# Kernel optimization log

Measured on AMD Instinct MI355X. Metric: run time of the kernel, lower is better.

Reference implementation:

```python
import jax, jax.numpy as jnp
import numpy as np

N_NODES = 50000   # hypergraph nodes
N_EDGES = 20000   # hyperedges
M = 400000        # node-edge incidences (node copies)
L = 800000        # inner GIN graph edges per side
HID = 128
IN_DIM = 128
B = 32            # graphs in batch
C = 10            # num_classes
N_LAYERS = 2
INNER = 2         # inner_num_layers
BN_EPS = 1e-5


def setup_inputs() -> dict:
    key = jax.random.key(0)
    ks = jax.random.split(key, 16)
    s = 0.05
    inp = {}
    inp["x_N"] = jax.random.normal(ks[0], (N_NODES, IN_DIM), jnp.float32)
    # embedding linear
    inp["We"] = jax.random.normal(ks[1], (IN_DIM, HID), jnp.float32) * s
    inp["be"] = jnp.zeros((HID,), jnp.float32)
    # GIN params: [outer_layer, direction(N2E/E2N), inner_conv, mlp_linear, hid, hid]
    inp["Wg"] = jax.random.normal(ks[2], (N_LAYERS, 2, INNER, 2, HID, HID), jnp.float32) * s
    inp["bg"] = jnp.zeros((N_LAYERS, 2, INNER, 2, HID), jnp.float32)
    inp["eps_g"] = jnp.zeros((N_LAYERS, 2, INNER), jnp.float32)
    # eval-mode BatchNorm affine params per inner conv
    inp["gamma"] = jnp.ones((N_LAYERS, 2, INNER, HID), jnp.float32)
    inp["beta"] = jnp.zeros((N_LAYERS, 2, INNER, HID), jnp.float32)
    # per-layer prediction heads
    inp["Wp"] = jax.random.normal(ks[3], (N_LAYERS + 1, HID, C), jnp.float32) * s
    inp["bp"] = jnp.zeros((N_LAYERS + 1, C), jnp.float32)
    # index tensors
    inp["ori_node_idx"] = jax.random.randint(ks[4], (M,), 0, N_NODES)
    inp["node2edge"] = jax.random.randint(ks[5], (M,), 0, N_EDGES)
    inp["edge_index_N"] = jax.random.randint(ks[6], (2, L), 0, M)
    inp["ori_edge_idx"] = jax.random.randint(ks[7], (M,), 0, N_EDGES)
    inp["edge2node"] = jax.random.randint(ks[8], (M,), 0, N_NODES)
    inp["edge_index_E"] = jax.random.randint(ks[9], (2, L), 0, M)
    inp["batch"] = jax.random.randint(ks[10], (M,), 0, B)
    return inp


def _gin(x, src, dst, Wg, bg, eps, gamma, beta):
    # GIN over the copy graph: h = MLP((1+eps)*x + sum_{j->i} x_j), BN (eval), ReLU between convs
    inv_std = 1.0 / jnp.sqrt(1.0 + BN_EPS)
    n = x.shape[0]
    for l in range(INNER):
        agg = jax.ops.segment_sum(x[src], dst, num_segments=n)
        h = (1.0 + eps[l]) * x + agg
        h = jax.nn.relu(h @ Wg[l, 0] + bg[l, 0])
        h = h @ Wg[l, 1] + bg[l, 1]
        h = gamma[l] * h * inv_std + beta[l]
        x = jax.nn.relu(h) if l < INNER - 1 else h
    return x


def reference(x_N, We, be, Wg, bg, eps_g, gamma, beta, Wp, bp,
              ori_node_idx, node2edge, edge_index_N,
              ori_edge_idx, edge2node, edge_index_E, batch):
    node_x = x_N @ We + be                       # [N, HID]
    xs = [node_x]
    for i in range(N_LAYERS):
        # node -> edge: gather copies, inner GIN, segment-sum pool over hyperedges
        nx = node_x[ori_node_idx]                # [M, HID]
        nx = _gin(nx, edge_index_N[0], edge_index_N[1],
                  Wg[i, 0], bg[i, 0], eps_g[i, 0], gamma[i, 0], beta[i, 0])
        edge_x = jax.ops.segment_sum(nx, node2edge, num_segments=N_EDGES)
        edge_x = jax.nn.relu(edge_x)             # EdgeUpdate (dropout off in eval)
        # edge -> node
        ex = edge_x[ori_edge_idx]                # [M, HID]
        ex = _gin(ex, edge_index_E[0], edge_index_E[1],
                  Wg[i, 1], bg[i, 1], eps_g[i, 1], gamma[i, 1], beta[i, 1])
        node_x = jax.ops.segment_sum(ex, edge2node, num_segments=N_NODES)
        node_x = jax.nn.relu(node_x)             # NodeUpdate
        xs.append(node_x)
    score = jnp.zeros((B, C), x_N.dtype)
    for i, x in enumerate(xs):
        pooled = jax.ops.segment_sum(x[ori_node_idx], batch, num_segments=B)
        score = score + pooled @ Wp[i] + bp[i]
    return score
```

## Files before the change

kernel.cpp:

```cpp
#include <hip/hip_runtime.h>
#include <hip/hip_bf16.h>

#define HID 128
static const int N_NODES = 50000;
static const int N_EDGES = 20000;
static const int M_COPIES = 400000;
static const int L_EDGES = 800000;
static const int NBATCH = 32;
static const int NCLS = 10;
#define INV_STD 0.9999950000374997f
#define IDX_CAP 384

typedef __attribute__((ext_vector_type(4))) float f32x4;
typedef __attribute__((ext_vector_type(8))) short short8;
typedef __attribute__((ext_vector_type(8))) unsigned short ushort8;
typedef __attribute__((ext_vector_type(4))) unsigned short u16x4;

__device__ __forceinline__ float bf2f(unsigned short u) {
    union { unsigned u; float f; } v; v.u = ((unsigned)u) << 16; return v.f;
}
__device__ __forceinline__ unsigned short f2bf(float f) {
    union { float f; unsigned u; } v; v.f = f;
    unsigned r = v.u + 0x7FFFu + ((v.u >> 16) & 1u);
    return (unsigned short)(r >> 16);
}
__device__ __forceinline__ void gatomic_add(float* p, float v) {
    unsafeAtomicAdd(p, v);
}

__device__ __forceinline__ unsigned short* xs_addr(unsigned short* Xs, int c, int r) {
    int byte = ((c * 64 + r) * 16) ^ ((c & 7) << 4);
    return (unsigned short*)((char*)Xs + byte);
}

__device__ __forceinline__ void stage8(const unsigned short* __restrict__ Wmat, int e,
                                       unsigned short* buf, int wave, int lane) {
    const char* g = (const char*)Wmat + ((size_t)e << 12) + (wave << 10) + (lane << 4);
    char* l = (char*)buf + (wave << 10);
    __builtin_amdgcn_global_load_lds(
        (const __attribute__((address_space(1))) unsigned int*)g,
        (__attribute__((address_space(3))) unsigned int*)l,
        16, 0, 0);
}

template<int N>
__device__ __forceinline__ void pipe_barrier() {
    if constexpr (N == 0) asm volatile("s_waitcnt vmcnt(0)" ::: "memory");
    else                  asm volatile("s_waitcnt vmcnt(1)" ::: "memory");
    __builtin_amdgcn_s_barrier();
    asm volatile("" ::: "memory");
}

__device__ __forceinline__ void mfma4(const unsigned short* Ws, const short8* xv,
                                      f32x4& a, int quad, int ln) {
#pragma unroll
    for (int kc = 0; kc < 4; ++kc) {
        short8 wa = *(const short8*)(Ws + (((kc * 4 + quad) * 16) + ln) * 8);
        a = __builtin_amdgcn_mfma_f32_16x16x32_bf16(wa, xv[kc], a, 0, 0, 0);
    }
}

__global__ __launch_bounds__(256) void prep_w(const float* __restrict__ We,
                                              const float* __restrict__ Wg,
                                              unsigned short* __restrict__ Wt) {
    int t = blockIdx.x * 256 + threadIdx.x;
    if (t >= 17 * 16384) return;
    int mat = t >> 14, rem = t & 16383;
    int h = rem >> 11, r2 = rem & 2047;
    int gg = r2 >> 7, r3 = r2 & 127;
    int n = r3 >> 3, j = r3 & 7;
    int k = gg * 8 + j, col = h * 16 + n;
    const float* src = (mat == 0) ? We : (Wg + (size_t)(mat - 1) * 16384);
    Wt[t] = f2bf(src[k * 128 + col]);
}

__global__ __launch_bounds__(256) void hist2_k(
    const int* __restrict__ iA, int nA, int* __restrict__ cA,
    const int* __restrict__ iB, int nB, int* __restrict__ cB) {
    int t = blockIdx.x * 256 + threadIdx.x;
    if (t < nA) atomicAdd(&cA[iA[t]], 1);
    if (t < nB) atomicAdd(&cB[iB[t]], 1);
}

__global__ __launch_bounds__(256) void scan1d_k(
    int* __restrict__ a0, int n0, int* __restrict__ p0,
    int* __restrict__ a1, int n1, int* __restrict__ p1) {
    int* a    = blockIdx.y ? a1 : a0;
    int n     = blockIdx.y ? n1 : n0;
    int* part = blockIdx.y ? p1 : p0;
    if ((int)(blockIdx.x * 256) >= n) return;
    __shared__ int s[256];
    int i = blockIdx.x * 256 + threadIdx.x;
    int v = (i < n) ? a[i] : 0;
    s[threadIdx.x] = v;
    __syncthreads();
#pragma unroll
    for (int d = 1; d < 256; d <<= 1) {
        int t = (threadIdx.x >= d) ? s[threadIdx.x - d] : 0;
        __syncthreads();
        s[threadIdx.x] += t;
        __syncthreads();
    }
    if (i < n) a[i] = s[threadIdx.x] - v;
    if (threadIdx.x == 255) part[blockIdx.x] = s[255];
}

__global__ __launch_bounds__(256) void scan2d_k(
    int* __restrict__ p0, int nb0, int* __restrict__ p1, int nb1) {
    int* part = blockIdx.x ? p1 : p0;
    int nb    = blockIdx.x ? nb1 : nb0;
    __shared__ int s[256];
    __shared__ int carry;
    if (threadIdx.x == 0) carry = 0;
    __syncthreads();
    for (int base = 0; base < nb; base += 256) {
        int i = base + threadIdx.x;
        int v = (i < nb) ? part[i] : 0;
        s[threadIdx.x] = v;
        __syncthreads();
#pragma unroll
        for (int d = 1; d < 256; d <<= 1) {
            int t = (threadIdx.x >= d) ? s[threadIdx.x - d] : 0;
            __syncthreads();
            s[threadIdx.x] += t;
            __syncthreads();
        }
        if (i < nb) part[i] = carry + s[threadIdx.x] - v;
        __syncthreads();
        if (threadIdx.x == 0) carry += s[255];
        __syncthreads();
    }
}

__global__ __launch_bounds__(256) void scan3d_k(
    int* __restrict__ a0, int n0, const int* __restrict__ p0,
    int* __restrict__ a1, int n1, const int* __restrict__ p1) {
    int* a          = blockIdx.y ? a1 : a0;
    int n           = blockIdx.y ? n1 : n0;
    const int* part = blockIdx.y ? p1 : p0;
    int i = blockIdx.x * 256 + threadIdx.x;
    if (i < n) a[i] += part[blockIdx.x];
}

__global__ __launch_bounds__(256) void fill_edge2_k(
    const int* __restrict__ sA, const int* __restrict__ dA, const int* __restrict__ rA,
    int nA, int* __restrict__ oA, int* __restrict__ ssA, int* __restrict__ ccA,
    const int* __restrict__ sB, const int* __restrict__ dB, const int* __restrict__ rB,
    int nB, int* __restrict__ oB, int* __restrict__ ssB, int* __restrict__ ccB) {
    int t = blockIdx.x * 256 + threadIdx.x;
    if (t < nA) {
        int d = dA[t]; int pos = atomicAdd(&oA[d], 1);
        int s = sA[t]; ssA[pos] = s; ccA[pos] = rA[s];
    }
    if (t < nB) {
        int d = dB[t]; int pos = atomicAdd(&oB[d], 1);
        int s = sB[t]; ssB[pos] = s; ccB[pos] = rB[s];
    }
}

__global__ __launch_bounds__(256) void fill_pool2_k(
    const int* __restrict__ gA, int nA, int* __restrict__ oA, int* __restrict__ itA,
    const int* __restrict__ gB, int nB, int* __restrict__ oB, int* __restrict__ itB) {
    int t = blockIdx.x * 256 + threadIdx.x;
    if (t < nA) { int pos = atomicAdd(&oA[gA[t]], 1); itA[pos] = t; }
    if (t < nB) { int pos = atomicAdd(&oB[gB[t]], 1); itB[pos] = t; }
}

__global__ __launch_bounds__(256) void segsum_pool(
    const unsigned short* __restrict__ tbl, const int* __restrict__ off,
    const int* __restrict__ items, unsigned short* __restrict__ out, int nseg)
{
    int wave = threadIdx.x >> 6, lane = threadIdx.x & 63;
    int seg = blockIdx.x * 4 + wave;
    if (seg >= nseg) return;
    int start = (seg == 0) ? 0 : off[seg - 1];
    int end = off[seg];
    int g = lane & 15, sub = lane >> 4;
    float a[8] = {0.f, 0.f, 0.f, 0.f, 0.f, 0.f, 0.f, 0.f};
    for (int p = start + sub; p < end; p += 4) {
        int r = items[p];
        ushort8 v = *(const ushort8*)(tbl + (size_t)r * 128 + g * 8);
#pragma unroll
        for (int j = 0; j < 8; ++j) a[j] += bf2f(v[j]);
    }
#pragma unroll
    for (int j = 0; j < 8; ++j) {
        a[j] += __shfl_xor(a[j], 16, 64);
        a[j] += __shfl_xor(a[j], 32, 64);
    }
    if (sub == 0) {
        ushort8 ov;
#pragma unroll
        for (int j = 0; j < 8; ++j) ov[j] = f2bf(fmaxf(a[j], 0.f));
        *(ushort8*)(out + (size_t)seg * 128 + g * 8) = ov;
    }
}

template<bool CONV0>
__global__ __launch_bounds__(256, 5) void fused_conv(
    const unsigned short* __restrict__ tbl,
    const int* __restrict__ self_idx,
    const int* __restrict__ off, const int* __restrict__ items,
    const float* __restrict__ eps_ptr,
    const unsigned short* __restrict__ W1t, const float* __restrict__ b1,
    const unsigned short* __restrict__ W2t, const float* __restrict__ b2,
    const float* __restrict__ gam, const float* __restrict__ bet,
    unsigned short* __restrict__ out)
{
    __shared__ __align__(16) unsigned short Xs[16 * 64 * 8];
    __shared__ __align__(16) unsigned short Wsb[3][2048];
    __shared__ int sIdx[IDX_CAP];
    __shared__ int meta[192];
    const int tid = threadIdx.x;
    const int row0 = blockIdx.x * 64;
    const int wave = tid >> 6, lane = tid & 63;

    stage8(W1t, 0, Wsb[0], wave, lane);
    stage8(W1t, 1, Wsb[1], wave, lane);

    const int bstart = (row0 == 0) ? 0 : off[row0 - 1];
    const int cnt = off[row0 + 63] - bstart;
    const bool useLds = (cnt <= IDX_CAP);

    if (tid == 0) sIdx[0] = 0;
    if (tid < 64) {
        int gr = row0 + tid;
        meta[tid]       = (gr == 0) ? 0 : off[gr - 1];
        meta[64 + tid]  = off[gr];
        meta[128 + tid] = CONV0 ? self_idx[gr] : gr;
    }
    if (useLds)
        for (int i = tid; i < cnt; i += 256) sIdx[i] = items[bstart + i];
    __syncthreads();

    const float e = 1.0f + eps_ptr[0];
    const int g = tid & 15;
    const int rb = tid >> 4;
    int st[4], en[4];
    float a[4][8];
#pragma unroll
    for (int i = 0; i < 4; ++i) {
        int r = rb + 16 * i;
        st[i] = meta[r]; en[i] = meta[64 + r];
        int self = meta[128 + r];
        ushort8 u = *(const ushort8*)(tbl + (size_t)self * 128 + g * 8);
#pragma unroll
        for (int j = 0; j < 8; ++j) a[i][j] = e * bf2f(u[j]);
    }
    if (useLds) {
        const int cmax = (cnt > 0) ? (cnt - 1) : 0;
#pragma unroll
        for (int i = 0; i < 4; ++i) { st[i] -= bstart; en[i] -= bstart; }
        while (__ballot((st[0] < en[0]) | (st[1] < en[1]) |
                        (st[2] < en[2]) | (st[3] < en[3]))) {
            ushort8 v[4];
#pragma unroll
            for (int i = 0; i < 4; ++i) {
                int p = st[i] < cmax ? st[i] : cmax;
                int idx = sIdx[p];
                v[i] = *(const ushort8*)(tbl + (size_t)idx * 128 + g * 8);
            }
#pragma unroll
            for (int i = 0; i < 4; ++i) {
                if (st[i] < en[i]) {
#pragma unroll
                    for (int j = 0; j < 8; ++j) a[i][j] += bf2f(v[i][j]);
                    st[i]++;
                }
            }
        }
    } else {
#pragma unroll
        for (int i = 0; i < 4; ++i) {
            for (int pos = st[i]; pos < en[i]; ++pos) {
                int rr = items[pos];
                ushort8 v = *(const ushort8*)(tbl + (size_t)rr * 128 + g * 8);
#pragma unroll
                for (int j = 0; j < 8; ++j) a[i][j] += bf2f(v[j]);
            }
        }
    }
#pragma unroll
    for (int i = 0; i < 4; ++i) {
        ushort8 xv;
#pragma unroll
        for (int j = 0; j < 8; ++j) xv[j] = f2bf(a[i][j]);
        *(ushort8*)xs_addr(Xs, g, rb + 16 * i) = xv;
    }
    __syncthreads();

    const int ln = lane & 15, quad = lane >> 4;
    const int row = wave * 16 + ln;

    short8 xb[4];
#pragma unroll
    for (int kc = 0; kc < 4; ++kc)
        xb[kc] = *(const short8*)xs_addr(Xs, kc * 4 + quad, row);

    f32x4 acc[8];
#pragma unroll
    for (int t = 0; t < 8; ++t) acc[t] = (f32x4){0.f, 0.f, 0.f, 0.f};

#pragma unroll
    for (int s = 0; s < 8; ++s) {
        int pf = s + 2;
        stage8(pf < 8 ? W1t : W2t, pf & 7, Wsb[pf % 3], wave, lane);
        mfma4(Wsb[s % 3], xb, acc[s], quad, ln);
        pipe_barrier<1>();
    }

    {
        const int j0 = (quad & 1) * 4;
#pragma unroll
        for (int t = 0; t < 8; ++t) {
            int p0 = t * 16 + quad * 4;
            f32x4 bv = *(const f32x4*)(b1 + p0);
            u16x4 hp;
#pragma unroll
            for (int i = 0; i < 4; ++i) hp[i] = f2bf(fmaxf(acc[t][i] + bv[i], 0.f));
            *(u16x4*)((char*)xs_addr(Xs, p0 >> 3, row) + j0 * 2) = hp;
        }
    }

    short8 hb[4];
#pragma unroll
    for (int kc = 0; kc < 4; ++kc)
        hb[kc] = *(const short8*)xs_addr(Xs, kc * 4 + quad, row);

#pragma unroll
    for (int t = 0; t < 8; ++t) acc[t] = (f32x4){0.f, 0.f, 0.f, 0.f};

#pragma unroll
    for (int f = 0; f < 8; ++f) {
        if (f < 6) stage8(W2t, f + 2, Wsb[(f + 10) % 3], wave, lane);
        mfma4(Wsb[(f + 8) % 3], hb, acc[f], quad, ln);
        if (f < 6)      pipe_barrier<1>();
        else if (f == 6) pipe_barrier<0>();
    }

    const int m = row0 + row;
#pragma unroll
    for (int t = 0; t < 8; ++t) {
        int n0 = t * 16 + quad * 4;
        f32x4 bv = *(const f32x4*)(b2 + n0);
        f32x4 gv = *(const f32x4*)(gam + n0);
        f32x4 tv = *(const f32x4*)(bet + n0);
        u16x4 op;
#pragma unroll
        for (int i = 0; i < 4; ++i) {
            float h = acc[t][i] + bv[i];
            h = gv[i] * h * INV_STD + tv[i];
            if (CONV0) h = fmaxf(h, 0.f);
            op[i] = f2bf(h);
        }
        *(u16x4*)(out + (size_t)m * 128 + n0) = op;
    }
}

__global__ __launch_bounds__(256) void gemm_embed(
    const float* __restrict__ in, const unsigned short* __restrict__ Wt,
    const float* __restrict__ bias, unsigned short* __restrict__ out_bf, int rows)
{
    __shared__ __align__(16) unsigned short Xs[16 * 64 * 8];
    __shared__ __align__(16) unsigned short Ws[16 * 128 * 8];
    int tid = threadIdx.x;
    int row0 = blockIdx.x * 64;
#pragma unroll
    for (int i = 0; i < 8; ++i) {
        int chunk = tid + i * 256;
        int n = chunk >> 4, g = chunk & 15;
        *(short8*)(Ws + (g * 128 + n) * 8) =
            *(const short8*)(Wt + (n >> 4) * 2048 + g * 128 + (n & 15) * 8);
    }
#pragma unroll
    for (int i = 0; i < 4; ++i) {
        int chunk = tid + i * 256;
        int r = chunk >> 4, g = chunk & 15;
        int gr = row0 + r;
        ushort8 v;
        if (gr < rows) {
            const float* p = in + (size_t)gr * 128 + g * 8;
            f32x4 a0 = *(const f32x4*)p;
            f32x4 a1 = *(const f32x4*)(p + 4);
#pragma unroll
            for (int j = 0; j < 4; ++j) { v[j] = f2bf(a0[j]); v[4 + j] = f2bf(a1[j]); }
        } else {
#pragma unroll
            for (int j = 0; j < 8; ++j) v[j] = 0;
        }
        *(ushort8*)(Xs + (g * 64 + r) * 8) = v;
    }
    __syncthreads();
    int wave = tid >> 6, lane = tid & 63;
    int m0 = wave * 16;
    int ln = lane & 15, quad = lane >> 4;
    f32x4 acc[8];
#pragma unroll
    for (int t = 0; t < 8; ++t) acc[t] = (f32x4){0.f, 0.f, 0.f, 0.f};
#pragma unroll
    for (int kc = 0; kc < 4; ++kc) {
        int g = kc * 4 + quad;
        short8 a = *(const short8*)(Xs + (g * 64 + m0 + ln) * 8);
#pragma unroll
        for (int t = 0; t < 8; ++t) {
            short8 b = *(const short8*)(Ws + (g * 128 + t * 16 + ln) * 8);
            acc[t] = __builtin_amdgcn_mfma_f32_16x16x32_bf16(a, b, acc[t], 0, 0, 0);
        }
    }
#pragma unroll
    for (int t = 0; t < 8; ++t) {
        int col = t * 16 + ln;
        float bi = bias[col];
#pragma unroll
        for (int i = 0; i < 4; ++i) {
            int gr = row0 + m0 + quad * 4 + i;
            if (gr < rows) out_bf[(size_t)gr * 128 + col] = f2bf(acc[t][i] + bi);
        }
    }
}

template<bool ACCUM>
__global__ __launch_bounds__(256) void proj_y(
    const unsigned short* __restrict__ nx, const float* __restrict__ Wp,
    float* __restrict__ y, int rows)
{
    __shared__ float Wl[HID * NCLS];
    for (int i = threadIdx.x; i < HID * NCLS; i += 256) Wl[i] = Wp[i];
    __syncthreads();
    int r = blockIdx.x * 256 + threadIdx.x;
    if (r >= rows) return;
    float acc[NCLS];
#pragma unroll
    for (int c = 0; c < NCLS; ++c) acc[c] = 0.f;
    const unsigned short* xp = nx + (size_t)r * 128;
#pragma unroll 4
    for (int g = 0; g < 16; ++g) {
        ushort8 u = *(const ushort8*)(xp + g * 8);
#pragma unroll
        for (int j = 0; j < 8; ++j) {
            float xv = bf2f(u[j]);
            const float* w = Wl + (g * 8 + j) * NCLS;
#pragma unroll
            for (int c = 0; c < NCLS; ++c) acc[c] += xv * w[c];
        }
    }
    float* yp = y + (size_t)r * NCLS;
#pragma unroll
    for (int c = 0; c < NCLS; ++c) {
        if (ACCUM) yp[c] += acc[c];
        else yp[c] = acc[c];
    }
}

__global__ __launch_bounds__(256) void score_scatter(
    const float* __restrict__ y, const int* __restrict__ ori,
    const int* __restrict__ batch, float* __restrict__ score)
{
    __shared__ float sc[NBATCH * NCLS];
    for (int i = threadIdx.x; i < NBATCH * NCLS; i += 256) sc[i] = 0.f;
    __syncthreads();
    int stride = gridDim.x * 256;
    for (int m = blockIdx.x * 256 + threadIdx.x; m < M_COPIES; m += stride) {
        int r = ori[m], b = batch[m];
        const float* yp = y + (size_t)r * NCLS;
#pragma unroll
        for (int c = 0; c < NCLS; ++c)
            __hip_atomic_fetch_add(&sc[b * NCLS + c], yp[c],
                                   __ATOMIC_RELAXED, __HIP_MEMORY_SCOPE_WORKGROUP);
    }
    __syncthreads();
    for (int i = threadIdx.x; i < NBATCH * NCLS; i += 256) gatomic_add(score + i, sc[i]);
}

__global__ void score_final(const float* __restrict__ score, const float* __restrict__ bp,
                            float* __restrict__ out)
{
    int t = threadIdx.x;
    if (t >= NBATCH * NCLS) return;
    int c = t % NCLS;
    out[t] = score[t] + bp[c] + bp[NCLS + c] + bp[2 * NCLS + c];
}

__global__ void fill_sentinel(float* out, int n, float enc) {
    int t = blockIdx.x * 64 + threadIdx.x;
    if (t < n) out[t] = enc;
}

extern "C" void kernel_launch(void* const* d_in, const int* in_sizes, int n_in,
                              void* d_out, int out_size, void* d_ws, size_t ws_size,
                              hipStream_t stream) {
    const float* x_N    = (const float*)d_in[0];
    const float* We     = (const float*)d_in[1];
    const float* be     = (const float*)d_in[2];
    const float* Wg     = (const float*)d_in[3];
    const float* bg     = (const float*)d_in[4];
    const float* eps_g  = (const float*)d_in[5];
    const float* gam    = (const float*)d_in[6];
    const float* bet    = (const float*)d_in[7];
    const float* Wp     = (const float*)d_in[8];
    const float* bp     = (const float*)d_in[9];
    const int* ori_node = (const int*)d_in[10];
    const int* node2edge= (const int*)d_in[11];
    const int* eiN      = (const int*)d_in[12];
    const int* ori_edge = (const int*)d_in[13];
    const int* edge2node= (const int*)d_in[14];
    const int* eiE      = (const int*)d_in[15];
    const int* batch    = (const int*)d_in[16];

    char* p = (char*)d_ws;
    auto take = [&](size_t n) { char* r = p; p += (n + 255) & ~(size_t)255; return r; };
    unsigned short* Wt  = (unsigned short*)take((size_t)17 * 16384 * 2);
    unsigned short* Xb  = (unsigned short*)take((size_t)M_COPIES * 128 * 2);
    unsigned short* Xb2 = (unsigned short*)take((size_t)M_COPIES * 128 * 2);
    unsigned short* nx  = (unsigned short*)take((size_t)N_NODES * 128 * 2);
    unsigned short* ex  = (unsigned short*)take((size_t)N_EDGES * 128 * 2);
    float* y            = (float*)take((size_t)N_NODES * NCLS * 4);
    float* score        = (float*)take((size_t)NBATCH * NCLS * 4);
    int* offN           = (int*)take((size_t)M_COPIES * 4);
    int* offE           = (int*)take((size_t)M_COPIES * 4);
    int* off_n2e        = (int*)take((size_t)N_EDGES * 4);
    int* off_e2n        = (int*)take((size_t)N_NODES * 4);
    int* srcsN          = (int*)take((size_t)L_EDGES * 4);
    int* compsN         = (int*)take((size_t)L_EDGES * 4);
    int* srcsE          = (int*)take((size_t)L_EDGES * 4);
    int* compsE         = (int*)take((size_t)L_EDGES * 4);
    int* it_n2e         = (int*)take((size_t)M_COPIES * 4);
    int* it_e2n         = (int*)take((size_t)M_COPIES * 4);
    int* part           = (int*)take((size_t)8192 * 4);
    size_t need = (size_t)(p - (char*)d_ws);
    if (need > ws_size) {
        fill_sentinel<<<(out_size + 63) / 64, 64, 0, stream>>>(
            (float*)d_out, out_size, 1.0e9f + (float)ws_size);
        return;
    }

    prep_w<<<1088, 256, 0, stream>>>(We, Wg, Wt);
    (void)hipMemsetAsync(score, 0, (size_t)NBATCH * NCLS * 4, stream);

    const int NB_M = (M_COPIES + 255) / 256;
    const int NB_L = (L_EDGES + 255) / 256;
    const int NB_N = (N_NODES + 255) / 256;
    int* partB = part + 4096;

    (void)hipMemsetAsync(offN, 0, (size_t)2 * M_COPIES * 4, stream);
    hist2_k<<<NB_L, 256, 0, stream>>>(eiN + L_EDGES, L_EDGES, offN,
                                      eiE + L_EDGES, L_EDGES, offE);
    scan1d_k<<<dim3(NB_M, 2), 256, 0, stream>>>(offN, M_COPIES, part, offE, M_COPIES, partB);
    scan2d_k<<<2, 256, 0, stream>>>(part, NB_M, partB, NB_M);
    scan3d_k<<<dim3(NB_M, 2), 256, 0, stream>>>(offN, M_COPIES, part, offE, M_COPIES, partB);
    fill_edge2_k<<<NB_L, 256, 0, stream>>>(eiN, eiN + L_EDGES, ori_node, L_EDGES, offN, srcsN, compsN,
                                           eiE, eiE + L_EDGES, ori_edge, L_EDGES, offE, srcsE, compsE);

    (void)hipMemsetAsync(off_n2e, 0,
        (size_t)((char*)off_e2n - (char*)off_n2e) + (size_t)N_NODES * 4, stream);
    hist2_k<<<NB_M, 256, 0, stream>>>(node2edge, M_COPIES, off_n2e,
                                      edge2node, M_COPIES, off_e2n);
    scan1d_k<<<dim3(NB_N, 2), 256, 0, stream>>>(off_n2e, N_EDGES, part, off_e2n, N_NODES, partB);
    scan2d_k<<<2, 256, 0, stream>>>(part, (N_EDGES + 255) / 256, partB, NB_N);
    scan3d_k<<<dim3(NB_N, 2), 256, 0, stream>>>(off_n2e, N_EDGES, part, off_e2n, N_NODES, partB);
    fill_pool2_k<<<NB_M, 256, 0, stream>>>(node2edge, M_COPIES, off_n2e, it_n2e,
                                           edge2node, M_COPIES, off_e2n, it_e2n);

    gemm_embed<<<(N_NODES + 63) / 64, 256, 0, stream>>>(x_N, Wt, be, nx, N_NODES);
    proj_y<false><<<(N_NODES + 255) / 256, 256, 0, stream>>>(nx, Wp, y, N_NODES);

    const int MBLK = M_COPIES / 64;
    for (int layer = 0; layer < 2; ++layer) {
        for (int dir = 0; dir < 2; ++dir) {
            int cj0 = layer * 4 + dir * 2;
            int cj1 = cj0 + 1;
            const unsigned short* base = (dir == 0) ? nx : ex;
            const int* selfI = (dir == 0) ? ori_node : ori_edge;
            const int* offD  = (dir == 0) ? offN : offE;
            const int* srcsD = (dir == 0) ? srcsN : srcsE;
            const int* compD = (dir == 0) ? compsN : compsE;

            fused_conv<true><<<MBLK, 256, 0, stream>>>(
                base, selfI, offD, compD, eps_g + cj0,
                Wt + (size_t)(1 + cj0 * 2) * 16384, bg + (cj0 * 2) * 128,
                Wt + (size_t)(1 + cj0 * 2 + 1) * 16384, bg + (cj0 * 2 + 1) * 128,
                gam + cj0 * 128, bet + cj0 * 128, Xb);
            fused_conv<false><<<MBLK, 256, 0, stream>>>(
                Xb, nullptr, offD, srcsD, eps_g + cj1,
                Wt + (size_t)(1 + cj1 * 2) * 16384, bg + (cj1 * 2) * 128,
                Wt + (size_t)(1 + cj1 * 2 + 1) * 16384, bg + (cj1 * 2 + 1) * 128,
                gam + cj1 * 128, bet + cj1 * 128, Xb2);
            if (dir == 0) {
                segsum_pool<<<(N_EDGES + 3) / 4, 256, 0, stream>>>(
                    Xb2, off_n2e, it_n2e, ex, N_EDGES);
            } else {
                segsum_pool<<<(N_NODES + 3) / 4, 256, 0, stream>>>(
                    Xb2, off_e2n, it_e2n, nx, N_NODES);
                proj_y<true><<<(N_NODES + 255) / 256, 256, 0, stream>>>(
                    nx, Wp + (layer + 1) * HID * NCLS, y, N_NODES);
            }
        }
    }
    score_scatter<<<256, 256, 0, stream>>>(y, ori_node, batch, score);
    score_final<<<1, 320, 0, stream>>>(score, bp, (float*)d_out);
}
```

Baseline: 1.418 ms.

## Bucket inner-GIN edges per 64-row block with packed src and row-local ids

Result: faster. 1.350 ms (-4.8%).

```diff
diff --git a/kernel.cpp b/kernel.cpp
--- a/kernel.cpp
+++ b/kernel.cpp
@@ -10,6 +10,8 @@
 static const int NCLS = 10;
 #define INV_STD 0.9999950000374997f
 #define IDX_CAP 384
+#define PKSHIFT 19
+#define PKMASK  0x7FFFF
 
 typedef __attribute__((ext_vector_type(4))) float f32x4;
 typedef __attribute__((ext_vector_type(8))) short short8;
@@ -76,10 +78,10 @@
 
 __global__ __launch_bounds__(256) void hist2_k(
     const int* __restrict__ iA, int nA, int* __restrict__ cA,
-    const int* __restrict__ iB, int nB, int* __restrict__ cB) {
+    const int* __restrict__ iB, int nB, int* __restrict__ cB, int shift) {
     int t = blockIdx.x * 256 + threadIdx.x;
-    if (t < nA) atomicAdd(&cA[iA[t]], 1);
-    if (t < nB) atomicAdd(&cB[iB[t]], 1);
+    if (t < nA) atomicAdd(&cA[iA[t] >> shift], 1);
+    if (t < nB) atomicAdd(&cB[iB[t] >> shift], 1);
 }
 
 __global__ __launch_bounds__(256) void scan1d_k(
@@ -142,19 +144,21 @@
     if (i < n) a[i] += part[blockIdx.x];
 }
 
-__global__ __launch_bounds__(256) void fill_edge2_k(
+__global__ __launch_bounds__(256) void fill_edgeblk2_k(
     const int* __restrict__ sA, const int* __restrict__ dA, const int* __restrict__ rA,
-    int nA, int* __restrict__ oA, int* __restrict__ ssA, int* __restrict__ ccA,
+    int nA, int* __restrict__ oA, int2* __restrict__ pkA,
     const int* __restrict__ sB, const int* __restrict__ dB, const int* __restrict__ rB,
-    int nB, int* __restrict__ oB, int* __restrict__ ssB, int* __restrict__ ccB) {
+    int nB, int* __restrict__ oB, int2* __restrict__ pkB) {
     int t = blockIdx.x * 256 + threadIdx.x;
     if (t < nA) {
-        int d = dA[t]; int pos = atomicAdd(&oA[d], 1);
-        int s = sA[t]; ssA[pos] = s; ccA[pos] = rA[s];
+        int d = dA[t]; int pos = atomicAdd(&oA[d >> 6], 1);
+        int s = sA[t]; int rl = (d & 63) << PKSHIFT;
+        pkA[pos] = (int2){rl | s, rl | rA[s]};
     }
     if (t < nB) {
-        int d = dB[t]; int pos = atomicAdd(&oB[d], 1);
-        int s = sB[t]; ssB[pos] = s; ccB[pos] = rB[s];
+        int d = dB[t]; int pos = atomicAdd(&oB[d >> 6], 1);
+        int s = sB[t]; int rl = (d & 63) << PKSHIFT;
+        pkB[pos] = (int2){rl | s, rl | rB[s]};
     }
 }
 
@@ -200,7 +204,7 @@
 __global__ __launch_bounds__(256, 5) void fused_conv(
     const unsigned short* __restrict__ tbl,
     const int* __restrict__ self_idx,
-    const int* __restrict__ off, const int* __restrict__ items,
+    const int* __restrict__ blkOff, const int2* __restrict__ edgePk,
     const float* __restrict__ eps_ptr,
     const unsigned short* __restrict__ W1t, const float* __restrict__ b1,
     const unsigned short* __restrict__ W2t, const float* __restrict__ b2,
@@ -210,7 +214,8 @@
     __shared__ __align__(16) unsigned short Xs[16 * 64 * 8];
     __shared__ __align__(16) unsigned short Wsb[3][2048];
     __shared__ int sIdx[IDX_CAP];
-    __shared__ int meta[192];
+    __shared__ int sSelf[64];
+    __shared__ int rcnt[64], rbase[64], rpos[64];
     const int tid = threadIdx.x;
     const int row0 = blockIdx.x * 64;
     const int wave = tid >> 6, lane = tid & 63;
@@ -218,39 +223,65 @@
     stage8(W1t, 0, Wsb[0], wave, lane);
     stage8(W1t, 1, Wsb[1], wave, lane);
 
-    const int bstart = (row0 == 0) ? 0 : off[row0 - 1];
-    const int cnt = off[row0 + 63] - bstart;
-    const bool useLds = (cnt <= IDX_CAP);
-
-    if (tid == 0) sIdx[0] = 0;
-    if (tid < 64) {
-        int gr = row0 + tid;
-        meta[tid]       = (gr == 0) ? 0 : off[gr - 1];
-        meta[64 + tid]  = off[gr];
-        meta[128 + tid] = CONV0 ? self_idx[gr] : gr;
-    }
-    if (useLds)
-        for (int i = tid; i < cnt; i += 256) sIdx[i] = items[bstart + i];
+    const int blk = blockIdx.x;
+    const int bstart = (blk == 0) ? 0 : blkOff[blk - 1];
+    const int cnt = blkOff[blk] - bstart;
+
+    if (tid < 64) sSelf[tid] = CONV0 ? self_idx[row0 + tid] : row0 + tid;
     __syncthreads();
 
     const float e = 1.0f + eps_ptr[0];
     const int g = tid & 15;
     const int rb = tid >> 4;
-    int st[4], en[4];
     float a[4][8];
 #pragma unroll
     for (int i = 0; i < 4; ++i) {
-        int r = rb + 16 * i;
-        st[i] = meta[r]; en[i] = meta[64 + r];
-        int self = meta[128 + r];
+        int self = sSelf[rb + 16 * i];
         ushort8 u = *(const ushort8*)(tbl + (size_t)self * 128 + g * 8);
 #pragma unroll
         for (int j = 0; j < 8; ++j) a[i][j] = e * bf2f(u[j]);
     }
-    if (useLds) {
-        const int cmax = (cnt > 0) ? (cnt - 1) : 0;
-#pragma unroll
-        for (int i = 0; i < 4; ++i) { st[i] -= bstart; en[i] -= bstart; }
+
+    int done = 0;
+    while (done < cnt) {
+        const int chunk = (cnt - done < IDX_CAP) ? (cnt - done) : IDX_CAP;
+        if (tid < 64) rcnt[tid] = 0;
+        __syncthreads();
+        int e0 = -1, e1 = -1;
+        if (tid < chunk) {
+            int2 pk = edgePk[bstart + done + tid];
+            e0 = CONV0 ? pk.y : pk.x;
+            atomicAdd(&rcnt[e0 >> PKSHIFT], 1);
+        }
+        if (tid + 256 < chunk) {
+            int2 pk = edgePk[bstart + done + tid + 256];
+            e1 = CONV0 ? pk.y : pk.x;
+            atomicAdd(&rcnt[e1 >> PKSHIFT], 1);
+        }
+        __syncthreads();
+        if (tid < 64) {
+            int c = rcnt[tid];
+            int s = c;
+#pragma unroll
+            for (int d = 1; d < 64; d <<= 1) {
+                int t = __shfl_up(s, d, 64);
+                if (tid >= d) s += t;
+            }
+            rbase[tid] = s - c;
+            rpos[tid]  = s - c;
+        }
+        __syncthreads();
+        if (e0 >= 0) { int p = atomicAdd(&rpos[e0 >> PKSHIFT], 1); sIdx[p] = e0 & PKMASK; }
+        if (e1 >= 0) { int p = atomicAdd(&rpos[e1 >> PKSHIFT], 1); sIdx[p] = e1 & PKMASK; }
+        __syncthreads();
+
+        int st[4], en[4];
+#pragma unroll
+        for (int i = 0; i < 4; ++i) {
+            int r = rb + 16 * i;
+            st[i] = rbase[r]; en[i] = rpos[r];
+        }
+        const int cmax = chunk - 1;
         while (__ballot((st[0] < en[0]) | (st[1] < en[1]) |
                         (st[2] < en[2]) | (st[3] < en[3]))) {
             ushort8 v[4];
@@ -269,17 +300,10 @@
                 }
             }
         }
-    } else {
-#pragma unroll
-        for (int i = 0; i < 4; ++i) {
-            for (int pos = st[i]; pos < en[i]; ++pos) {
-                int rr = items[pos];
-                ushort8 v = *(const ushort8*)(tbl + (size_t)rr * 128 + g * 8);
-#pragma unroll
-                for (int j = 0; j < 8; ++j) a[i][j] += bf2f(v[j]);
-            }
-        }
-    }
+        done += chunk;
+        __syncthreads();
+    }
+
 #pragma unroll
     for (int i = 0; i < 4; ++i) {
         ushort8 xv;
@@ -507,6 +531,8 @@
     const int* eiE      = (const int*)d_in[15];
     const int* batch    = (const int*)d_in[16];
 
+    const int NBLK = M_COPIES / 64;
+
     char* p = (char*)d_ws;
     auto take = [&](size_t n) { char* r = p; p += (n + 255) & ~(size_t)255; return r; };
     unsigned short* Wt  = (unsigned short*)take((size_t)17 * 16384 * 2);
@@ -516,14 +542,12 @@
     unsigned short* ex  = (unsigned short*)take((size_t)N_EDGES * 128 * 2);
     float* y            = (float*)take((size_t)N_NODES * NCLS * 4);
     float* score        = (float*)take((size_t)NBATCH * NCLS * 4);
-    int* offN           = (int*)take((size_t)M_COPIES * 4);
-    int* offE           = (int*)take((size_t)M_COPIES * 4);
+    int* blkN           = (int*)take((size_t)2 * NBLK * 4);
+    int* blkE           = blkN + NBLK;
     int* off_n2e        = (int*)take((size_t)N_EDGES * 4);
     int* off_e2n        = (int*)take((size_t)N_NODES * 4);
-    int* srcsN          = (int*)take((size_t)L_EDGES * 4);
-    int* compsN         = (int*)take((size_t)L_EDGES * 4);
-    int* srcsE          = (int*)take((size_t)L_EDGES * 4);
-    int* compsE         = (int*)take((size_t)L_EDGES * 4);
+    int2* pkN           = (int2*)take((size_t)L_EDGES * 8);
+    int2* pkE           = (int2*)take((size_t)L_EDGES * 8);
     int* it_n2e         = (int*)take((size_t)M_COPIES * 4);
     int* it_e2n         = (int*)take((size_t)M_COPIES * 4);
     int* part           = (int*)take((size_t)8192 * 4);
@@ -540,21 +564,23 @@
     const int NB_M = (M_COPIES + 255) / 256;
     const int NB_L = (L_EDGES + 255) / 256;
     const int NB_N = (N_NODES + 255) / 256;
+    const int NB_B = (NBLK + 255) / 256;
     int* partB = part + 4096;
 
-    (void)hipMemsetAsync(offN, 0, (size_t)2 * M_COPIES * 4, stream);
-    hist2_k<<<NB_L, 256, 0, stream>>>(eiN + L_EDGES, L_EDGES, offN,
-                                      eiE + L_EDGES, L_EDGES, offE);
-    scan1d_k<<<dim3(NB_M, 2), 256, 0, stream>>>(offN, M_COPIES, part, offE, M_COPIES, partB);
-    scan2d_k<<<2, 256, 0, stream>>>(part, NB_M, partB, NB_M);
-    scan3d_k<<<dim3(NB_M, 2), 256, 0, stream>>>(offN, M_COPIES, part, offE, M_COPIES, partB);
-    fill_edge2_k<<<NB_L, 256, 0, stream>>>(eiN, eiN + L_EDGES, ori_node, L_EDGES, offN, srcsN, compsN,
-                                           eiE, eiE + L_EDGES, ori_edge, L_EDGES, offE, srcsE, compsE);
+    (void)hipMemsetAsync(blkN, 0, (size_t)2 * NBLK * 4, stream);
+    hist2_k<<<NB_L, 256, 0, stream>>>(eiN + L_EDGES, L_EDGES, blkN,
+                                      eiE + L_EDGES, L_EDGES, blkE, 6);
+    scan1d_k<<<dim3(NB_B, 2), 256, 0, stream>>>(blkN, NBLK, part, blkE, NBLK, partB);
+    scan2d_k<<<2, 256, 0, stream>>>(part, NB_B, partB, NB_B);
+    scan3d_k<<<dim3(NB_B, 2), 256, 0, stream>>>(blkN, NBLK, part, blkE, NBLK, partB);
+    fill_edgeblk2_k<<<NB_L, 256, 0, stream>>>(
+        eiN, eiN + L_EDGES, ori_node, L_EDGES, blkN, pkN,
+        eiE, eiE + L_EDGES, ori_edge, L_EDGES, blkE, pkE);
 
     (void)hipMemsetAsync(off_n2e, 0,
         (size_t)((char*)off_e2n - (char*)off_n2e) + (size_t)N_NODES * 4, stream);
     hist2_k<<<NB_M, 256, 0, stream>>>(node2edge, M_COPIES, off_n2e,
-                                      edge2node, M_COPIES, off_e2n);
+                                      edge2node, M_COPIES, off_e2n, 0);
     scan1d_k<<<dim3(NB_N, 2), 256, 0, stream>>>(off_n2e, N_EDGES, part, off_e2n, N_NODES, partB);
     scan2d_k<<<2, 256, 0, stream>>>(part, (N_EDGES + 255) / 256, partB, NB_N);
     scan3d_k<<<dim3(NB_N, 2), 256, 0, stream>>>(off_n2e, N_EDGES, part, off_e2n, N_NODES, partB);
@@ -564,24 +590,22 @@
     gemm_embed<<<(N_NODES + 63) / 64, 256, 0, stream>>>(x_N, Wt, be, nx, N_NODES);
     proj_y<false><<<(N_NODES + 255) / 256, 256, 0, stream>>>(nx, Wp, y, N_NODES);
 
-    const int MBLK = M_COPIES / 64;
     for (int layer = 0; layer < 2; ++layer) {
         for (int dir = 0; dir < 2; ++dir) {
             int cj0 = layer * 4 + dir * 2;
             int cj1 = cj0 + 1;
             const unsigned short* base = (dir == 0) ? nx : ex;
             const int* selfI = (dir == 0) ? ori_node : ori_edge;
-            const int* offD  = (dir == 0) ? offN : offE;
-            const int* srcsD = (dir == 0) ? srcsN : srcsE;
-            const int* compD = (dir == 0) ? compsN : compsE;
-
-            fused_conv<true><<<MBLK, 256, 0, stream>>>(
-                base, selfI, offD, compD, eps_g + cj0,
+            const int* blkD  = (dir == 0) ? blkN : blkE;
+            const int2* pkD  = (dir == 0) ? pkN : pkE;
+
+            fused_conv<true><<<NBLK, 256, 0, stream>>>(
+                base, selfI, blkD, pkD, eps_g + cj0,
                 Wt + (size_t)(1 + cj0 * 2) * 16384, bg + (cj0 * 2) * 128,
                 Wt + (size_t)(1 + cj0 * 2 + 1) * 16384, bg + (cj0 * 2 + 1) * 128,
                 gam + cj0 * 128, bet + cj0 * 128, Xb);
-            fused_conv<false><<<MBLK, 256, 0, stream>>>(
-                Xb, nullptr, offD, srcsD, eps_g + cj1,
+            fused_conv<false><<<NBLK, 256, 0, stream>>>(
+                Xb, nullptr, blkD, pkD, eps_g + cj1,
                 Wt + (size_t)(1 + cj1 * 2) * 16384, bg + (cj1 * 2) * 128,
                 Wt + (size_t)(1 + cj1 * 2 + 1) * 16384, bg + (cj1 * 2 + 1) * 128,
                 gam + cj1 * 128, bet + cj1 * 128, Xb2);
```
